# Kernel tuning notes

Hardware: AMD Instinct MI355X
Metric: run time of the kernel (lower is better)

Reference implementation:

```python
import jax, jax.numpy as jnp
import numpy as np

H = 1024  # hidden_size


def _lstm_layer(x, w_ih, w_hh, b_ih, b_hh):
    # x: [S, B, I] -> outputs [S, B, H]
    S, B, _ = x.shape
    # Precompute input projection for all timesteps (both biases folded in,
    # matching gi + gh where gi carries b_ih and gh carries b_hh).
    gi = jnp.einsum('sbi,gi->sbg', x, w_ih) + b_ih + b_hh  # [S, B, 4H]
    h0 = jnp.zeros((B, H), x.dtype)
    c0 = jnp.zeros((B, H), x.dtype)

    def step(carry, gi_t):
        h, c = carry
        gates = gi_t + h @ w_hh.T                # [B, 4H]
        i, f, g, o = jnp.split(gates, 4, axis=1)  # gate order: i, f, g, o
        c_new = jax.nn.sigmoid(f) * c + jax.nn.sigmoid(i) * jnp.tanh(g)
        h_new = jax.nn.sigmoid(o) * jnp.tanh(c_new)
        return (h_new, c_new), h_new

    (h_last, c_last), ys = jax.lax.scan(step, (h0, c0), gi)
    return ys, h_last, c_last


def setup_inputs() -> dict:
    key = jax.random.key(0)
    ks = jax.random.split(key, 6)
    S, B, I = 512, 64, 1024
    def xavier(k, shape):
        fan_out, fan_in = shape
        lim = np.sqrt(6.0 / (fan_in + fan_out)).astype(np.float32)
        return jax.random.uniform(k, shape, jnp.float32, -lim, lim)
    return {
        'x': jax.random.normal(ks[0], (S, B, I), jnp.float32),
        'w_ih_0': xavier(ks[1], (4 * H, I)),
        'w_hh_0': xavier(ks[2], (4 * H, H)),
        'b_ih_0': jnp.zeros((4 * H,), jnp.float32),
        'b_hh_0': jnp.zeros((4 * H,), jnp.float32),
        'w_ih_1': xavier(ks[3], (4 * H, H)),
        'w_hh_1': xavier(ks[4], (4 * H, H)),
        'b_ih_1': jnp.zeros((4 * H,), jnp.float32),
        'b_hh_1': jnp.zeros((4 * H,), jnp.float32),
    }


def reference(x, w_ih_0, w_hh_0, b_ih_0, b_hh_0, w_ih_1, w_hh_1, b_ih_1, b_hh_1):
    # 2-layer unidirectional LSTM, dropout=0, batch_first=False, zero init state.
    y0, h0, c0 = _lstm_layer(x, w_ih_0, w_hh_0, b_ih_0, b_hh_0)
    y1, h1, c1 = _lstm_layer(y0, w_ih_1, w_hh_1, b_ih_1, b_hh_1)
    h_n = jnp.stack([h0, h1], axis=0)  # [num_layers, B, H]
    c_n = jnp.stack([c0, c1], axis=0)
    return y1, h_n, c_n
```

## Files before the change

kernel.cpp:

```cpp
#include <hip/hip_runtime.h>

typedef __attribute__((ext_vector_type(8))) short short8;
typedef __attribute__((ext_vector_type(4))) float f32x4;
typedef unsigned int uint32;
typedef unsigned long long u64;

#define OFF_GI    0ull
#define OFF_XB    268435456ull
#define OFF_WIH0  335544320ull
#define OFF_WPKI  343932928ull
#define OFF_WPK0  352321536ull
#define OFF_WPK1  360710144ull
#define OFF_B0    369098752ull
#define OFF_B1    369115136ull
#define OFF_CNT   369131520ull
#define OFF_HBUF  369164288ull
#define WS_REQUIRED 369426432ull

#define ALOAD(p)    __hip_atomic_load((p), __ATOMIC_RELAXED, __HIP_MEMORY_SCOPE_AGENT)
#define ASTOREV(p,v) __hip_atomic_store((p), (v), __ATOMIC_RELAXED, __HIP_MEMORY_SCOPE_AGENT)
#define AADD(p,v)   __hip_atomic_fetch_add((p), (v), __ATOMIC_RELAXED, __HIP_MEMORY_SCOPE_AGENT)
#define WD_ITERS 30000

__device__ __forceinline__ unsigned short f2bf(float f) {
    union { float f; uint32 u; } v; v.f = f;
    uint32 u = v.u + 0x7FFFu + ((v.u >> 16) & 1u);
    return (unsigned short)(u >> 16);
}
__device__ __forceinline__ float bf2f(unsigned short u) {
    union { uint32 u; float f; } v; v.u = ((uint32)u) << 16; return v.f;
}
__device__ __forceinline__ float sigmoidf_(float x) {
    return 1.0f / (1.0f + __expf(-x));
}
__device__ __forceinline__ float tanhf_(float x) {
    return 1.0f - 2.0f / (1.0f + __expf(2.0f * x));
}

__global__ void diag_kernel(float* out, float val) {
    if (blockIdx.x == 0 && threadIdx.x == 0) out[0] = val;
}

__global__ void cast_bf16_kernel(const float* __restrict__ in,
                                 unsigned short* __restrict__ out, int n4) {
    int i = blockIdx.x * 256 + threadIdx.x;
    if (i < n4) {
        float4 v = ((const float4*)in)[i];
        ushort4 o;
        o.x = f2bf(v.x); o.y = f2bf(v.y); o.z = f2bf(v.z); o.w = f2bf(v.w);
        ((ushort4*)out)[i] = o;
    }
}

__global__ void bias_sum_kernel(const float* __restrict__ a,
                                const float* __restrict__ b,
                                float* __restrict__ o, int n) {
    int i = blockIdx.x * 256 + threadIdx.x;
    if (i < n) o[i] = a[i] + b[i];
}

__global__ void bias_perm_kernel(const float* __restrict__ a,
                                 const float* __restrict__ b,
                                 float* __restrict__ o) {
    int i = blockIdx.x * 256 + threadIdx.x;
    int c = i >> 2, g = i & 3;
    o[i] = a[g * 1024 + c] + b[g * 1024 + c];
}

__global__ void pack_whh_kernel(const float* __restrict__ whh,
                                unsigned short* __restrict__ out) {
    int o = blockIdx.x * 256 + threadIdx.x;
    int j  = o & 7;
    int l  = (o >> 3) & 63;
    int f  = (o >> 9) & 31;
    int wq = o >> 14;
    int w = wq >> 2, q = wq & 3;
    int g = f >> 3,  s = f & 7;
    int n = g * 1024 + w * 16 + (l & 15);
    int k = q * 256 + s * 32 + ((l >> 4)) * 8 + j;
    out[o] = f2bf(whh[(size_t)n * 1024 + k]);
}

__global__ void pack_wih1_frag_kernel(const float* __restrict__ wih1,
                                      unsigned short* __restrict__ out) {
    int o = blockIdx.x * 256 + threadIdx.x;
    int j  = o & 7;
    int l  = (o >> 3) & 63;
    int ks = (o >> 9) & 31;
    int wq = o >> 14;
    int w = wq >> 2, q = wq & 3;
    int np = w * 64 + q * 16 + (l & 15);
    int c = np >> 2, g = np & 3;
    int k = ks * 32 + ((l >> 4)) * 8 + j;
    out[o] = f2bf(wih1[(size_t)(g * 1024 + c) * 1024 + k]);
}

__global__ __launch_bounds__(256, 2) void gemm_bt_kernel(
    const unsigned short* __restrict__ A,
    const unsigned short* __restrict__ B,
    const float* __restrict__ bias,
    unsigned short* __restrict__ C) {
    __shared__ __align__(16) unsigned short As[128 * 64];
    __shared__ __align__(16) unsigned short Bs[128 * 64];
    const int tid = threadIdx.x;
    const int l = tid & 63;
    const int wv = tid >> 6;
    const int wm = wv >> 1, wn = wv & 1;
    const long bm = blockIdx.x, bn = blockIdx.y;

    f32x4 acc[4][4];
#pragma unroll
    for (int i = 0; i < 4; ++i)
#pragma unroll
        for (int j = 0; j < 4; ++j)
            acc[i][j] = (f32x4){0.f, 0.f, 0.f, 0.f};

    for (int k0 = 0; k0 < 1024; k0 += 64) {
#pragma unroll
        for (int ii = 0; ii < 4; ++ii) {
            int slot = ii * 256 + tid;
            int row = slot >> 3, csw = slot & 7;
            int cc = csw ^ (row & 7);
            *(uint4*)&As[slot * 8] =
                *(const uint4*)(A + (bm * 128 + row) * 1024 + k0 + cc * 8);
            *(uint4*)&Bs[slot * 8] =
                *(const uint4*)(B + (bn * 128 + row) * 1024 + k0 + cc * 8);
        }
        __syncthreads();
#pragma unroll
        for (int s = 0; s < 2; ++s) {
            short8 af[4], bfm[4];
#pragma unroll
            for (int i = 0; i < 4; ++i) {
                int row = wm * 64 + i * 16 + (l & 15);
                af[i] = *(const short8*)&As[(row * 8 + (((s * 4) + (l >> 4)) ^ (row & 7))) * 8];
            }
#pragma unroll
            for (int j = 0; j < 4; ++j) {
                int row = wn * 64 + j * 16 + (l & 15);
                bfm[j] = *(const short8*)&Bs[(row * 8 + (((s * 4) + (l >> 4)) ^ (row & 7))) * 8];
            }
#pragma unroll
            for (int i = 0; i < 4; ++i)
#pragma unroll
                for (int j = 0; j < 4; ++j)
                    acc[i][j] = __builtin_amdgcn_mfma_f32_16x16x32_bf16(
                        af[i], bfm[j], acc[i][j], 0, 0, 0);
        }
        __syncthreads();
    }
#pragma unroll
    for (int j = 0; j < 4; ++j) {
        float bj = bias[bn * 128 + wn * 64 + j * 16 + (l & 15)];
#pragma unroll
        for (int i = 0; i < 4; ++i) {
#pragma unroll
            for (int r = 0; r < 4; ++r) {
                long row = bm * 128 + wm * 64 + i * 16 + (l >> 4) * 4 + r;
                C[row * 4096 + bn * 128 + wn * 64 + j * 16 + (l & 15)] =
                    f2bf(acc[i][j][r] + bj);
            }
        }
    }
}

__device__ __forceinline__ void gi1_tile(
    const unsigned short* hs,
    const unsigned short* __restrict__ wpkI,
    const float* __restrict__ b1p,
    unsigned short* gi1,
    int tg, int p, int w, int q, int l)
{
    f32x4 gacc = (f32x4){0.f, 0.f, 0.f, 0.f};
    const int arow = l & 15;
    const unsigned short* wb = wpkI + (size_t)(w * 4 + q) * 16384 + (size_t)l * 8;
#pragma unroll 4
    for (int ks = 0; ks < 32; ++ks) {
        short8 bfk = *(const short8*)(wb + ks * 512);
        short8 afk = *(const short8*)&hs[(arow * 128 + ((ks * 4 + (l >> 4)) ^ (arow & 7))) * 8];
        gacc = __builtin_amdgcn_mfma_f32_16x16x32_bf16(afk, bfk, gacc, 0, 0, 0);
    }
    const int colp = w * 64 + q * 16 + (l & 15);
    float bj = b1p[colp];
#pragma unroll
    for (int r = 0; r < 4; ++r) {
        int v0 = f2bf(gacc[r] + bj);
        int v1 = __shfl_down(v0, 1);
        int v2 = __shfl_down(v0, 2);
        int v3 = __shfl_down(v0, 3);
        if ((l & 3) == 0) {
            size_t row = (size_t)tg * 64 + p * 16 + (l >> 4) * 4 + r;
            u64 u = (u64)(v0 & 0xffff) | ((u64)(v1 & 0xffff) << 16) |
                    ((u64)(v2 & 0xffff) << 32) | ((u64)(v3 & 0xffff) << 48);
            *(u64*)(gi1 + row * 4096 + colp) = u;
        }
    }
}

template <int LAYER>
__global__ __launch_bounds__(256, 2) void lstm_rec_kernel(
    unsigned short* gi,
    const unsigned short* __restrict__ wpk,
    const unsigned short* __restrict__ wpkI,
    const float* __restrict__ b1p,
    unsigned short* hbuf,
    float* __restrict__ yf,
    float* __restrict__ hn, float* __restrict__ cn,
    int* cnt) {
    __shared__ __align__(16) unsigned short hs[16 * 1024];
    __shared__ float red[4][4][16][16];
    const int tid = threadIdx.x;
    const int l = tid & 63, q = tid >> 6;
    const int W = blockIdx.x;
    const int p = W >> 6, w = W & 63;
    int* cg = cnt + p * 2048;

    short8 bfr[4][8];
    {
        const unsigned short* wb = wpk + (size_t)((w * 4 + q) * 32) * 512 + (size_t)l * 8;
#pragma unroll
        for (int g = 0; g < 4; ++g)
#pragma unroll
            for (int s = 0; s < 8; ++s)
                bfr[g][s] = *(const short8*)(wb + (g * 8 + s) * 512);
    }

    float c_state = 0.0f;
    const int be = tid >> 4, je = tid & 15;
    const int hrow = p * 16 + be;
    const int hcol = w * 16 + je;

    for (int t = 0; t < 512; ++t) {
        float g0, g1, g2, g3;
        if (LAYER == 0) {
            const unsigned short* gp = gi + (size_t)t * 262144 + (size_t)hrow * 4096 + hcol;
            g0 = bf2f(gp[0]);
            g1 = bf2f(gp[1024]);
            g2 = bf2f(gp[2048]);
            g3 = bf2f(gp[3072]);
        } else {
            u64 gv = *(const u64*)(gi + ((size_t)t * 64 + hrow) * 4096 + (size_t)hcol * 4);
            g0 = bf2f((unsigned short)gv);
            g1 = bf2f((unsigned short)(gv >> 16));
            g2 = bf2f((unsigned short)(gv >> 32));
            g3 = bf2f((unsigned short)(gv >> 48));
        }

        if (t > 0 && tid == 0) {
            int iters = 0;
            while (ALOAD(&cg[t - 1]) < 64) {
                __builtin_amdgcn_s_sleep(2);
                if (++iters > WD_ITERS) break;
            }
        }
        __syncthreads();

        {
            const u64* hp64 = (const u64*)(hbuf + (size_t)(t & 1) * 65536);
#pragma unroll
            for (int ii = 0; ii < 8; ++ii) {
                int slot = ii * 256 + tid;
                int row = slot >> 7, cs = slot & 127;
                int cc = cs ^ (row & 7);
                size_t gidx = ((size_t)(p * 16 + row) * 1024 + (size_t)cc * 8) >> 2;
                u64 lo = ALOAD(&hp64[gidx]);
                u64 hi = ALOAD(&hp64[gidx + 1]);
                *(u64*)&hs[slot * 8]     = lo;
                *(u64*)&hs[slot * 8 + 4] = hi;
            }
        }
        __syncthreads();

        f32x4 acc[4];
#pragma unroll
        for (int g = 0; g < 4; ++g) acc[g] = (f32x4){0.f, 0.f, 0.f, 0.f};
        const int arow = l & 15;
#pragma unroll
        for (int s = 0; s < 8; ++s) {
            int chunk = q * 32 + s * 4 + (l >> 4);
            short8 af = *(const short8*)&hs[(arow * 128 + (chunk ^ (arow & 7))) * 8];
#pragma unroll
            for (int g = 0; g < 4; ++g)
                acc[g] = __builtin_amdgcn_mfma_f32_16x16x32_bf16(
                    af, bfr[g][s], acc[g], 0, 0, 0);
        }
#pragma unroll
        for (int g = 0; g < 4; ++g)
#pragma unroll
            for (int r = 0; r < 4; ++r)
                red[q][g][(l >> 4) * 4 + r][l & 15] = acc[g][r];
        __syncthreads();

        float gate_i = g0, gate_f = g1, gate_g = g2, gate_o = g3;
#pragma unroll
        for (int qq = 0; qq < 4; ++qq) {
            gate_i += red[qq][0][be][je];
            gate_f += red[qq][1][be][je];
            gate_g += red[qq][2][be][je];
            gate_o += red[qq][3][be][je];
        }
        float ig = sigmoidf_(gate_i);
        float fg = sigmoidf_(gate_f);
        float gg = tanhf_(gate_g);
        float og = sigmoidf_(gate_o);
        c_state = fg * c_state + ig * gg;
        float h_new = og * tanhf_(c_state);

        unsigned short hb = f2bf(h_new);
        {
            int v0 = hb;
            int v1 = __shfl_down(v0, 1);
            int v2 = __shfl_down(v0, 2);
            int v3 = __shfl_down(v0, 3);
            if ((l & 3) == 0) {
                u64 u = (u64)(v0 & 0xffff) | ((u64)(v1 & 0xffff) << 16) |
                        ((u64)(v2 & 0xffff) << 32) | ((u64)(v3 & 0xffff) << 48);
                u64* dst = (u64*)(hbuf + (size_t)((t + 1) & 1) * 65536 +
                                  (size_t)hrow * 1024 + hcol);
                ASTOREV(dst, u);
            }
        }
        if (yf) yf[(size_t)t * 65536 + (size_t)hrow * 1024 + hcol] = h_new;
        if (t == 511) {
            hn[(size_t)hrow * 1024 + hcol] = h_new;
            cn[(size_t)hrow * 1024 + hcol] = c_state;
        }
        __syncthreads();
        if (tid == 0) AADD(&cg[t], 1);

        if (LAYER == 0 && t > 0) {
            gi1_tile(hs, wpkI, b1p, gi, t - 1, p, w, q, l);
        }
    }

    if (LAYER == 0) {
        if (tid == 0) {
            int iters = 0;
            while (ALOAD(&cg[511]) < 64) {
                __builtin_amdgcn_s_sleep(2);
                if (++iters > WD_ITERS) break;
            }
        }
        __syncthreads();
        {
            const u64* hp64 = (const u64*)hbuf;
#pragma unroll
            for (int ii = 0; ii < 8; ++ii) {
                int slot = ii * 256 + tid;
                int row = slot >> 7, cs = slot & 127;
                int cc = cs ^ (row & 7);
                size_t gidx = ((size_t)(p * 16 + row) * 1024 + (size_t)cc * 8) >> 2;
                u64 lo = ALOAD(&hp64[gidx]);
                u64 hi = ALOAD(&hp64[gidx + 1]);
                *(u64*)&hs[slot * 8]     = lo;
                *(u64*)&hs[slot * 8 + 4] = hi;
            }
        }
        __syncthreads();
        gi1_tile(hs, wpkI, b1p, gi, 511, p, w, q, l);
    }
}

extern "C" void kernel_launch(void* const* d_in, const int* in_sizes, int n_in,
                              void* d_out, int out_size, void* d_ws, size_t ws_size,
                              hipStream_t stream) {
    const float* x    = (const float*)d_in[0];
    const float* wih0 = (const float*)d_in[1];
    const float* whh0 = (const float*)d_in[2];
    const float* bih0 = (const float*)d_in[3];
    const float* bhh0 = (const float*)d_in[4];
    const float* wih1 = (const float*)d_in[5];
    const float* whh1 = (const float*)d_in[6];
    const float* bih1 = (const float*)d_in[7];
    const float* bhh1 = (const float*)d_in[8];
    float* out = (float*)d_out;

    if (ws_size < WS_REQUIRED) {
        diag_kernel<<<1, 64, 0, stream>>>(out, (float)(ws_size >> 20));
        return;
    }

    char* ws = (char*)d_ws;
    unsigned short* gi    = (unsigned short*)(ws + OFF_GI);
    unsigned short* xb    = (unsigned short*)(ws + OFF_XB);
    unsigned short* wih0b = (unsigned short*)(ws + OFF_WIH0);
    unsigned short* wpkI  = (unsigned short*)(ws + OFF_WPKI);
    unsigned short* wpk0  = (unsigned short*)(ws + OFF_WPK0);
    unsigned short* wpk1  = (unsigned short*)(ws + OFF_WPK1);
    float*          b0    = (float*)(ws + OFF_B0);
    float*          b1p   = (float*)(ws + OFF_B1);
    int*            cnt   = (int*)(ws + OFF_CNT);
    unsigned short* hbuf  = (unsigned short*)(ws + OFF_HBUF);

    cast_bf16_kernel<<<32768, 256, 0, stream>>>(x, xb, 8388608);
    cast_bf16_kernel<<<4096, 256, 0, stream>>>(wih0, wih0b, 1048576);
    pack_wih1_frag_kernel<<<16384, 256, 0, stream>>>(wih1, wpkI);
    pack_whh_kernel<<<16384, 256, 0, stream>>>(whh0, wpk0);
    pack_whh_kernel<<<16384, 256, 0, stream>>>(whh1, wpk1);
    bias_sum_kernel<<<16, 256, 0, stream>>>(bih0, bhh0, b0, 4096);
    bias_perm_kernel<<<16, 256, 0, stream>>>(bih1, bhh1, b1p);

    gemm_bt_kernel<<<dim3(256, 32), 256, 0, stream>>>(xb, wih0b, b0, gi);

    hipMemsetAsync(cnt, 0, 32768 + 262144, stream);
    lstm_rec_kernel<0><<<256, 256, 0, stream>>>(gi, wpk0, wpkI, b1p, hbuf,
                                                nullptr,
                                                out + 33554432, out + 33685504,
                                                cnt);
    hipMemsetAsync(cnt, 0, 32768 + 262144, stream);
    lstm_rec_kernel<1><<<256, 256, 0, stream>>>(gi, wpk1, wpkI, b1p, hbuf,
                                                out,
                                                out + 33554432 + 65536,
                                                out + 33685504 + 65536,
                                                cnt);
}
```

Before: 5.674 ms.

## Split layer-1 input projection into separate producer blocks overlapping layer-0 recurrence

Layer 0 is launched with 512 blocks: the first 256 run the recurrence and the other 256 compute the layer-1 input-projection tiles. The projection blocks wait on per-step completion counters, and a new counter stops the recurrent blocks from overwriting the double-buffered h before it has been consumed. This takes the gi1 GEMM off the recurrent critical path. In exchange it adds another spin-wait dependency between the two block groups and requires all 512 blocks to be co-resident (launch bounds allow two per CU). If they are not all resident, the counter waits would stall until the watchdog breaks them.

After: 5.998 ms. +5.7%, slower.

```diff
diff --git a/kernel.cpp b/kernel.cpp
--- a/kernel.cpp
+++ b/kernel.cpp
@@ -197,12 +197,181 @@
     }
 }
 
-template <int LAYER>
-__global__ __launch_bounds__(256, 2) void lstm_rec_kernel(
+__global__ __launch_bounds__(256, 2) void lstm_l0_fused_kernel(
     unsigned short* gi,
-    const unsigned short* __restrict__ wpk,
+    const unsigned short* __restrict__ wpk0,
     const unsigned short* __restrict__ wpkI,
     const float* __restrict__ b1p,
+    unsigned short* hbuf,
+    float* __restrict__ hn, float* __restrict__ cn,
+    int* cnt)
+{
+    __shared__ __align__(16) char smem[49152];
+    const int bid = blockIdx.x;
+    const int tid = threadIdx.x;
+    const int l = tid & 63, q = tid >> 6;
+
+    if (bid < 256) {
+        unsigned short* hs = (unsigned short*)smem;
+        float (*red)[4][16][16] = (float (*)[4][16][16])(smem + 32768);
+        const int p = bid >> 6, w = bid & 63;
+        int* cg = cnt + p * 2048;
+        int* pr = cnt + p * 2048 + 1024;
+
+        short8 bfr[4][8];
+        {
+            const unsigned short* wb = wpk0 + (size_t)((w * 4 + q) * 32) * 512 + (size_t)l * 8;
+#pragma unroll
+            for (int g = 0; g < 4; ++g)
+#pragma unroll
+                for (int s = 0; s < 8; ++s)
+                    bfr[g][s] = *(const short8*)(wb + (g * 8 + s) * 512);
+        }
+
+        float c_state = 0.0f;
+        const int be = tid >> 4, je = tid & 15;
+        const int hrow = p * 16 + be;
+        const int hcol = w * 16 + je;
+
+        for (int t = 0; t < 512; ++t) {
+            const unsigned short* gp = gi + (size_t)t * 262144 + (size_t)hrow * 4096 + hcol;
+            float g0 = bf2f(gp[0]);
+            float g1 = bf2f(gp[1024]);
+            float g2 = bf2f(gp[2048]);
+            float g3 = bf2f(gp[3072]);
+
+            if (tid == 0) {
+                if (t > 0) {
+                    int iters = 0;
+                    while (ALOAD(&cg[t - 1]) < 64) {
+                        __builtin_amdgcn_s_sleep(2);
+                        if (++iters > WD_ITERS) break;
+                    }
+                }
+                if (t >= 2) {
+                    int iters = 0;
+                    while (ALOAD(&pr[t - 2]) < 64) {
+                        __builtin_amdgcn_s_sleep(2);
+                        if (++iters > WD_ITERS) break;
+                    }
+                }
+            }
+            __syncthreads();
+
+            {
+                const u64* hp64 = (const u64*)(hbuf + (size_t)(t & 1) * 65536);
+#pragma unroll
+                for (int ii = 0; ii < 8; ++ii) {
+                    int slot = ii * 256 + tid;
+                    int row = slot >> 7, cs = slot & 127;
+                    int cc = cs ^ (row & 7);
+                    size_t gidx = ((size_t)(p * 16 + row) * 1024 + (size_t)cc * 8) >> 2;
+                    u64 lo = ALOAD(&hp64[gidx]);
+                    u64 hi = ALOAD(&hp64[gidx + 1]);
+                    *(u64*)&hs[slot * 8]     = lo;
+                    *(u64*)&hs[slot * 8 + 4] = hi;
+                }
+            }
+            __syncthreads();
+
+            f32x4 acc[4];
+#pragma unroll
+            for (int g = 0; g < 4; ++g) acc[g] = (f32x4){0.f, 0.f, 0.f, 0.f};
+            const int arow = l & 15;
+#pragma unroll
+            for (int s = 0; s < 8; ++s) {
+                int chunk = q * 32 + s * 4 + (l >> 4);
+                short8 af = *(const short8*)&hs[(arow * 128 + (chunk ^ (arow & 7))) * 8];
+#pragma unroll
+                for (int g = 0; g < 4; ++g)
+                    acc[g] = __builtin_amdgcn_mfma_f32_16x16x32_bf16(
+                        af, bfr[g][s], acc[g], 0, 0, 0);
+            }
+#pragma unroll
+            for (int g = 0; g < 4; ++g)
+#pragma unroll
+                for (int r = 0; r < 4; ++r)
+                    red[q][g][(l >> 4) * 4 + r][l & 15] = acc[g][r];
+            __syncthreads();
+
+            float gate_i = g0, gate_f = g1, gate_g = g2, gate_o = g3;
+#pragma unroll
+            for (int qq = 0; qq < 4; ++qq) {
+                gate_i += red[qq][0][be][je];
+                gate_f += red[qq][1][be][je];
+                gate_g += red[qq][2][be][je];
+                gate_o += red[qq][3][be][je];
+            }
+            float ig = sigmoidf_(gate_i);
+            float fg = sigmoidf_(gate_f);
+            float gg = tanhf_(gate_g);
+            float og = sigmoidf_(gate_o);
+            c_state = fg * c_state + ig * gg;
+            float h_new = og * tanhf_(c_state);
+
+            unsigned short hb = f2bf(h_new);
+            {
+                int v0 = hb;
+                int v1 = __shfl_down(v0, 1);
+                int v2 = __shfl_down(v0, 2);
+                int v3 = __shfl_down(v0, 3);
+                if ((l & 3) == 0) {
+                    u64 u = (u64)(v0 & 0xffff) | ((u64)(v1 & 0xffff) << 16) |
+                            ((u64)(v2 & 0xffff) << 32) | ((u64)(v3 & 0xffff) << 48);
+                    u64* dst = (u64*)(hbuf + (size_t)((t + 1) & 1) * 65536 +
+                                      (size_t)hrow * 1024 + hcol);
+                    ASTOREV(dst, u);
+                }
+            }
+            if (t == 511) {
+                hn[(size_t)hrow * 1024 + hcol] = h_new;
+                cn[(size_t)hrow * 1024 + hcol] = c_state;
+            }
+            __syncthreads();
+            if (tid == 0) AADD(&cg[t], 1);
+        }
+    } else {
+        unsigned short* hs = (unsigned short*)smem;
+        const int W = bid - 256;
+        const int p = W >> 6, w = W & 63;
+        int* cg = cnt + p * 2048;
+        int* pr = cnt + p * 2048 + 1024;
+
+        for (int t = 0; t < 512; ++t) {
+            if (tid == 0) {
+                int iters = 0;
+                while (ALOAD(&cg[t]) < 64) {
+                    __builtin_amdgcn_s_sleep(2);
+                    if (++iters > WD_ITERS) break;
+                }
+            }
+            __syncthreads();
+
+            {
+                const u64* hp64 = (const u64*)(hbuf + (size_t)((t + 1) & 1) * 65536);
+#pragma unroll
+                for (int ii = 0; ii < 8; ++ii) {
+                    int slot = ii * 256 + tid;
+                    int row = slot >> 7, cs = slot & 127;
+                    int cc = cs ^ (row & 7);
+                    size_t gidx = ((size_t)(p * 16 + row) * 1024 + (size_t)cc * 8) >> 2;
+                    u64 lo = ALOAD(&hp64[gidx]);
+                    u64 hi = ALOAD(&hp64[gidx + 1]);
+                    *(u64*)&hs[slot * 8]     = lo;
+                    *(u64*)&hs[slot * 8 + 4] = hi;
+                }
+            }
+            __syncthreads();
+            if (tid == 0) AADD(&pr[t], 1);
+
+            gi1_tile(hs, wpkI, b1p, gi, t, p, w, q, l);
+        }
+    }
+}
+
+__global__ __launch_bounds__(256, 2) void lstm_rec1_kernel(
+    const unsigned short* __restrict__ gi,
+    const unsigned short* __restrict__ wpk,
     unsigned short* hbuf,
     float* __restrict__ yf,
     float* __restrict__ hn, float* __restrict__ cn,
@@ -231,20 +400,11 @@
     const int hcol = w * 16 + je;
 
     for (int t = 0; t < 512; ++t) {
-        float g0, g1, g2, g3;
-        if (LAYER == 0) {
-            const unsigned short* gp = gi + (size_t)t * 262144 + (size_t)hrow * 4096 + hcol;
-            g0 = bf2f(gp[0]);
-            g1 = bf2f(gp[1024]);
-            g2 = bf2f(gp[2048]);
-            g3 = bf2f(gp[3072]);
-        } else {
-            u64 gv = *(const u64*)(gi + ((size_t)t * 64 + hrow) * 4096 + (size_t)hcol * 4);
-            g0 = bf2f((unsigned short)gv);
-            g1 = bf2f((unsigned short)(gv >> 16));
-            g2 = bf2f((unsigned short)(gv >> 32));
-            g3 = bf2f((unsigned short)(gv >> 48));
-        }
+        u64 gv = *(const u64*)(gi + ((size_t)t * 64 + hrow) * 4096 + (size_t)hcol * 4);
+        float g0 = bf2f((unsigned short)gv);
+        float g1 = bf2f((unsigned short)(gv >> 16));
+        float g2 = bf2f((unsigned short)(gv >> 32));
+        float g3 = bf2f((unsigned short)(gv >> 48));
 
         if (t > 0 && tid == 0) {
             int iters = 0;
@@ -320,44 +480,13 @@
                 ASTOREV(dst, u);
             }
         }
-        if (yf) yf[(size_t)t * 65536 + (size_t)hrow * 1024 + hcol] = h_new;
+        yf[(size_t)t * 65536 + (size_t)hrow * 1024 + hcol] = h_new;
         if (t == 511) {
             hn[(size_t)hrow * 1024 + hcol] = h_new;
             cn[(size_t)hrow * 1024 + hcol] = c_state;
         }
         __syncthreads();
         if (tid == 0) AADD(&cg[t], 1);
-
-        if (LAYER == 0 && t > 0) {
-            gi1_tile(hs, wpkI, b1p, gi, t - 1, p, w, q, l);
-        }
-    }
-
-    if (LAYER == 0) {
-        if (tid == 0) {
-            int iters = 0;
-            while (ALOAD(&cg[511]) < 64) {
-                __builtin_amdgcn_s_sleep(2);
-                if (++iters > WD_ITERS) break;
-            }
-        }
-        __syncthreads();
-        {
-            const u64* hp64 = (const u64*)hbuf;
-#pragma unroll
-            for (int ii = 0; ii < 8; ++ii) {
-                int slot = ii * 256 + tid;
-                int row = slot >> 7, cs = slot & 127;
-                int cc = cs ^ (row & 7);
-                size_t gidx = ((size_t)(p * 16 + row) * 1024 + (size_t)cc * 8) >> 2;
-                u64 lo = ALOAD(&hp64[gidx]);
-                u64 hi = ALOAD(&hp64[gidx + 1]);
-                *(u64*)&hs[slot * 8]     = lo;
-                *(u64*)&hs[slot * 8 + 4] = hi;
-            }
-        }
-        __syncthreads();
-        gi1_tile(hs, wpkI, b1p, gi, 511, p, w, q, l);
     }
 }
 
@@ -403,14 +532,12 @@
     gemm_bt_kernel<<<dim3(256, 32), 256, 0, stream>>>(xb, wih0b, b0, gi);
 
     hipMemsetAsync(cnt, 0, 32768 + 262144, stream);
-    lstm_rec_kernel<0><<<256, 256, 0, stream>>>(gi, wpk0, wpkI, b1p, hbuf,
-                                                nullptr,
-                                                out + 33554432, out + 33685504,
-                                                cnt);
+    lstm_l0_fused_kernel<<<512, 256, 0, stream>>>(gi, wpk0, wpkI, b1p, hbuf,
+                                                  out + 33554432, out + 33685504,
+                                                  cnt);
     hipMemsetAsync(cnt, 0, 32768 + 262144, stream);
-    lstm_rec_kernel<1><<<256, 256, 0, stream>>>(gi, wpk1, wpkI, b1p, hbuf,
-                                                out,
-                                                out + 33554432 + 65536,
-                                                out + 33685504 + 65536,
-                                                cnt);
-}
+    lstm_rec1_kernel<<<256, 256, 0, stream>>>(gi, wpk1, hbuf, out,
+                                              out + 33554432 + 65536,
+                                              out + 33685504 + 65536,
+                                              cnt);
+}
```
